# Performance work log

Measured on AMD Instinct MI355X. Metric: run time of the kernel, lower is better.

Reference implementation:

```python
import jax, jax.numpy as jnp
import numpy as np

E = 600_000
NUM_RADIAL = 6
HIDDEN = 128
OUT = 256
NUM_LAYERS = 3
N_NODES = 50_000


def setup_inputs() -> dict:
    key = jax.random.key(0)
    ks = jax.random.split(key, 6)
    x = jax.random.normal(ks[0], (E, HIDDEN), dtype=jnp.float32)
    rbf = jax.random.normal(ks[1], (E, NUM_RADIAL), dtype=jnp.float32)
    i = jax.random.randint(ks[2], (E,), 0, N_NODES, dtype=jnp.int64)
    # Linear weights stored as [in, out] so y = x @ W (equivalent to torch x @ W.T)
    W_rbf = jax.random.normal(ks[3], (NUM_RADIAL, HIDDEN), dtype=jnp.float32) / np.sqrt(NUM_RADIAL)
    W_down = jax.random.normal(ks[4], (HIDDEN, OUT), dtype=jnp.float32) / np.sqrt(HIDDEN)
    Ws = jax.random.normal(ks[5], (NUM_LAYERS, OUT, OUT), dtype=jnp.float32) / np.sqrt(OUT)
    bs = jnp.zeros((NUM_LAYERS, OUT), dtype=jnp.float32)
    return {"x": x, "rbf": rbf, "i": i, "W_rbf": W_rbf, "W_down": W_down,
            "Ws": Ws, "bs": bs, "num_nodes": N_NODES}


def reference(x, rbf, i, W_rbf, W_down, Ws, bs, num_nodes):
    # elementwise gate: lin_rbf(rbf) * x  -> [E, hidden]
    g = (rbf @ W_rbf) * x
    # scatter-add over edge target index i -> [num_nodes, hidden]
    h = jax.ops.segment_sum(g, i, num_segments=num_nodes)
    # down projection -> [num_nodes, out]
    h = h @ W_down
    # dense MLP stack with SiLU
    for k in range(Ws.shape[0]):
        h = jax.nn.silu(h @ Ws[k] + bs[k])
    return h
```

## Files before the change

### kernel.cpp

```cpp
#include <hip/hip_runtime.h>
#include <hip/hip_bf16.h>
#include <cstdint>

typedef __attribute__((ext_vector_type(8))) short short8;
typedef __attribute__((ext_vector_type(4))) float floatx4;

#define HIDDEN 128
#define NOUT 256

__global__ __launch_bounds__(256) void prep_weights(
    const float* __restrict__ Wd, const float* __restrict__ Ws,
    __hip_bfloat16* __restrict__ WdT, __hip_bfloat16* __restrict__ WsT)
{
    int tid = blockIdx.x * 256 + threadIdx.x;
    if (tid < 256 * 128) {
        int n = tid >> 7, k = tid & 127;
        WdT[tid] = __float2bfloat16(Wd[k * 256 + n]);
    }
    int tid2 = tid - 256 * 128;
    if (tid2 >= 0 && tid2 < 3 * 256 * 256) {
        int l = tid2 >> 16;
        int rem = tid2 & 65535;
        int n = rem >> 8, k = rem & 255;
        WsT[tid2] = __float2bfloat16(Ws[l * 65536 + k * 256 + n]);
    }
}

__global__ __launch_bounds__(256) void hist_k(
    const int* __restrict__ idx, int* __restrict__ cnt, int E)
{
    int e = blockIdx.x * 256 + threadIdx.x;
    if (e < E) atomicAdd(&cnt[idx[e]], 1);
}

__global__ __launch_bounds__(256) void scan_blocksum_k(
    const int* __restrict__ cnt, int* __restrict__ blocksum, int M)
{
    int base = blockIdx.x * 1024;
    int t = threadIdx.x;
    int s = 0;
#pragma unroll
    for (int j = 0; j < 4; ++j) {
        int p = base + t * 4 + j;
        if (p < M) s += cnt[p];
    }
#pragma unroll
    for (int d = 32; d > 0; d >>= 1) s += __shfl_down(s, d);
    __shared__ int wsum[4];
    if ((t & 63) == 0) wsum[t >> 6] = s;
    __syncthreads();
    if (t == 0) blocksum[blockIdx.x] = wsum[0] + wsum[1] + wsum[2] + wsum[3];
}

__global__ __launch_bounds__(64) void scan_base_k(
    const int* __restrict__ blocksum, int* __restrict__ blockbase,
    int* __restrict__ offsets, int nb, int M)
{
    int lane = threadIdx.x;
    int carry = 0;
    for (int base = 0; base < nb; base += 64) {
        int v = (base + lane < nb) ? blocksum[base + lane] : 0;
        int incl = v;
#pragma unroll
        for (int d = 1; d < 64; d <<= 1) {
            int u = __shfl_up(incl, d);
            if (lane >= d) incl += u;
        }
        if (base + lane < nb) blockbase[base + lane] = carry + incl - v;
        carry += __shfl(incl, 63);
    }
    if (lane == 0) offsets[M] = carry;
}

__global__ __launch_bounds__(256) void scan_offsets_k(
    const int* __restrict__ cnt, const int* __restrict__ blockbase,
    int* __restrict__ offsets, int* __restrict__ cursor, int M)
{
    int base = blockIdx.x * 1024;
    int t = threadIdx.x, lane = t & 63, wv = t >> 6;
    int v[4];
    int s = 0;
#pragma unroll
    for (int j = 0; j < 4; ++j) {
        int p = base + t * 4 + j;
        v[j] = (p < M) ? cnt[p] : 0;
        s += v[j];
    }
    int incl = s;
#pragma unroll
    for (int d = 1; d < 64; d <<= 1) {
        int u = __shfl_up(incl, d);
        if (lane >= d) incl += u;
    }
    __shared__ int wtot[4];
    if (lane == 63) wtot[wv] = incl;
    __syncthreads();
    int wbase = 0;
    for (int j = 0; j < wv; ++j) wbase += wtot[j];
    int start = blockbase[blockIdx.x] + wbase + incl - s;
#pragma unroll
    for (int j = 0; j < 4; ++j) {
        int p = base + t * 4 + j;
        if (p < M) { offsets[p] = start; cursor[p] = start; }
        start += v[j];
    }
}

__global__ __launch_bounds__(256) void fill_k(
    const int* __restrict__ idx, int* __restrict__ cursor,
    int* __restrict__ edge_ids, int E)
{
    int e = blockIdx.x * 256 + threadIdx.x;
    if (e < E) {
        int pos = atomicAdd(&cursor[idx[e]], 1);
        edge_ids[pos] = e;
    }
}

__global__ __launch_bounds__(256) void gather_k(
    const float* __restrict__ x, const float* __restrict__ rbf,
    const float* __restrict__ Wrbf, const int* __restrict__ offsets,
    const int* __restrict__ edge_ids, __hip_bfloat16* __restrict__ hacc, int M)
{
    int t = threadIdx.x;
    int wave = t >> 6, lane = t & 63;
    int n = blockIdx.x * 4 + wave;
    if (n >= M) return;

    int c0 = lane * 2;
    float w0[6], w1[6];
#pragma unroll
    for (int r = 0; r < 6; ++r) {
        w0[r] = Wrbf[r * HIDDEN + c0];
        w1[r] = Wrbf[r * HIDDEN + c0 + 1];
    }

    int s = offsets[n], eend = offsets[n + 1];
    float a0 = 0.f, a1 = 0.f;

    for (int p = s; p < eend; p += 64) {
        int nb = eend - p;
        if (nb > 64) nb = 64;
        int eid = (p + lane < eend) ? edge_ids[p + lane] : 0;

        int j = 0;
        for (; j + 4 <= nb; j += 4) {
#pragma unroll
            for (int u = 0; u < 4; ++u) {
                int e = __builtin_amdgcn_readlane(eid, j + u);
                const float* rb = rbf + (long)e * 6;
                float2 xv = *(const float2*)&x[(long)e * HIDDEN + c0];
                float p0 = 0.f, p1 = 0.f;
#pragma unroll
                for (int r = 0; r < 6; ++r) {
                    float rv = rb[r];
                    p0 += rv * w0[r];
                    p1 += rv * w1[r];
                }
                a0 += p0 * xv.x;
                a1 += p1 * xv.y;
            }
        }
        for (; j < nb; ++j) {
            int e = __builtin_amdgcn_readlane(eid, j);
            const float* rb = rbf + (long)e * 6;
            float2 xv = *(const float2*)&x[(long)e * HIDDEN + c0];
            float p0 = 0.f, p1 = 0.f;
#pragma unroll
            for (int r = 0; r < 6; ++r) {
                float rv = rb[r];
                p0 += rv * w0[r];
                p1 += rv * w1[r];
            }
            a0 += p0 * xv.x;
            a1 += p1 * xv.y;
        }
    }

    __hip_bfloat162 pk;
    pk.x = __float2bfloat16(a0);
    pk.y = __float2bfloat16(a1);
    *(__hip_bfloat162*)&hacc[(long)n * HIDDEN + c0] = pk;
}

__global__ __launch_bounds__(256, 3) void mlp_fused(
    const __hip_bfloat16* __restrict__ hacc, const __hip_bfloat16* __restrict__ WdT,
    const __hip_bfloat16* __restrict__ WsT, const float* __restrict__ bs,
    float* __restrict__ out, int M)
{
    __shared__ __hip_bfloat16 Al[64][264];

    int t = threadIdx.x;
    int lane = t & 63, w = t >> 6;
    int q = lane >> 4, r16 = lane & 15;
    int m0 = blockIdx.x * 64;

#pragma unroll
    for (int it = 0; it < 4; ++it) {
        int idx = it * 256 + t;
        int row = idx >> 4;
        int col = (idx & 15) * 8;
        int gr = m0 + row; if (gr >= M) gr = M - 1;
        *(short8*)&Al[row][col] = *(const short8*)&hacc[(long)gr * HIDDEN + col];
    }
    __syncthreads();

    for (int layer = 0; layer < 4; ++layer) {
        const int K = (layer == 0) ? 128 : 256;
        const __hip_bfloat16* BT = (layer == 0) ? WdT : WsT + (layer - 1) * 65536;
        const __hip_bfloat16* Brow = BT + (long)(w * 64 + r16) * K;

        floatx4 acc[4][4] = {};
        short8 bcur[4], bnxt[4];
#pragma unroll
        for (int nt = 0; nt < 4; ++nt)
            bcur[nt] = *(const short8*)&Brow[(long)nt * 16 * K + q * 8];

        for (int kk = 0; kk < K; kk += 32) {
            short8 af[4];
#pragma unroll
            for (int mt = 0; mt < 4; ++mt)
                af[mt] = *(const short8*)&Al[mt * 16 + r16][kk + q * 8];
            int kn = kk + 32;
            if (kn < K) {
#pragma unroll
                for (int nt = 0; nt < 4; ++nt)
                    bnxt[nt] = *(const short8*)&Brow[(long)nt * 16 * K + kn + q * 8];
            }
#pragma unroll
            for (int mt = 0; mt < 4; ++mt)
#pragma unroll
                for (int nt = 0; nt < 4; ++nt)
                    acc[mt][nt] = __builtin_amdgcn_mfma_f32_16x16x32_bf16(
                        af[mt], bcur[nt], acc[mt][nt], 0, 0, 0);
#pragma unroll
            for (int nt = 0; nt < 4; ++nt) bcur[nt] = bnxt[nt];
        }

        if (layer < 3) {
            __syncthreads();
            const float* bias = (layer == 0) ? nullptr : bs + (layer - 1) * 256;
#pragma unroll
            for (int mt = 0; mt < 4; ++mt) {
#pragma unroll
                for (int rr = 0; rr < 4; ++rr) {
                    int row = mt * 16 + q * 4 + rr;
#pragma unroll
                    for (int nt = 0; nt < 4; ++nt) {
                        int col = w * 64 + nt * 16 + r16;
                        float v = acc[mt][nt][rr];
                        if (layer > 0) { v += bias[col]; v = v / (1.f + __expf(-v)); }
                        Al[row][col] = __float2bfloat16(v);
                    }
                }
            }
            __syncthreads();
        } else {
            const float* bias = bs + 2 * 256;
#pragma unroll
            for (int mt = 0; mt < 4; ++mt) {
#pragma unroll
                for (int rr = 0; rr < 4; ++rr) {
                    int row = m0 + mt * 16 + q * 4 + rr;
                    if (row < M) {
#pragma unroll
                        for (int nt = 0; nt < 4; ++nt) {
                            int col = w * 64 + nt * 16 + r16;
                            float v = acc[mt][nt][rr] + bias[col];
                            v = v / (1.f + __expf(-v));
                            out[(long)row * NOUT + col] = v;
                        }
                    }
                }
            }
        }
    }
}

extern "C" void kernel_launch(void* const* d_in, const int* in_sizes, int n_in,
                              void* d_out, int out_size, void* d_ws, size_t ws_size,
                              hipStream_t stream)
{
    const float* x    = (const float*)d_in[0];
    const float* rbf  = (const float*)d_in[1];
    const int*   idx  = (const int*)d_in[2];
    const float* Wrbf = (const float*)d_in[3];
    const float* Wd   = (const float*)d_in[4];
    const float* Ws   = (const float*)d_in[5];
    const float* bs   = (const float*)d_in[6];

    int E = in_sizes[0] / HIDDEN;
    int M = out_size / NOUT;
    int nb = (M + 1023) / 1024;

    char* ws = (char*)d_ws;
    __hip_bfloat16* hacc = (__hip_bfloat16*)ws;
    size_t off = (size_t)M * HIDDEN * sizeof(float);
    __hip_bfloat16* WdT = (__hip_bfloat16*)(ws + off); off += 256 * 128 * 2;
    __hip_bfloat16* WsT = (__hip_bfloat16*)(ws + off); off += 3 * 256 * 256 * 2;
    int* cnt       = (int*)(ws + off); off += (size_t)M * 4;
    int* offsets   = (int*)(ws + off); off += (size_t)(M + 1) * 4;
    int* cursor    = (int*)(ws + off); off += (size_t)M * 4;
    int* edge_ids  = (int*)(ws + off); off += (size_t)E * 4;
    int* blocksum  = (int*)(ws + off); off += (size_t)nb * 4;
    int* blockbase = (int*)(ws + off); off += (size_t)nb * 4;

    hipMemsetAsync(cnt, 0, (size_t)M * sizeof(int), stream);
    prep_weights<<<(256 * 128 + 3 * 256 * 256 + 255) / 256, 256, 0, stream>>>(Wd, Ws, WdT, WsT);
    hist_k<<<(E + 255) / 256, 256, 0, stream>>>(idx, cnt, E);
    scan_blocksum_k<<<nb, 256, 0, stream>>>(cnt, blocksum, M);
    scan_base_k<<<1, 64, 0, stream>>>(blocksum, blockbase, offsets, nb, M);
    scan_offsets_k<<<nb, 256, 0, stream>>>(cnt, blockbase, offsets, cursor, M);
    fill_k<<<(E + 255) / 256, 256, 0, stream>>>(idx, cursor, edge_ids, E);
    gather_k<<<(M + 3) / 4, 256, 0, stream>>>(x, rbf, Wrbf, offsets, edge_ids, hacc, M);
    mlp_fused<<<(M + 63) / 64, 256, 0, stream>>>(hacc, WdT, WsT, bs, (float*)d_out, M);
}
```

Measured before the change: 629.7 us.

## Fuse CSR build and gather into one persistent cooperative kernel

Replaces the memset plus seven separate front-end kernels (weight prep, histogram, three-stage scan, fill, gather) with a single cooperative persistent kernel that separates phases with grid-wide syncs. The goal is to remove per-launch gaps and tail idle time between the many small kernels. In exchange, grid.sync barriers are added, occupancy is capped by the grid size, and the gather becomes a grid-stride loop over nodes. The old multi-kernel path stays as a fallback if the cooperative launch fails.

Result: slower. 1.394 ms (+121.4%).

```diff
diff --git a/kernel.cpp b/kernel.cpp
--- a/kernel.cpp
+++ b/kernel.cpp
@@ -1,12 +1,181 @@
 #include <hip/hip_runtime.h>
 #include <hip/hip_bf16.h>
+#include <hip/hip_cooperative_groups.h>
 #include <cstdint>
+
+namespace cg = cooperative_groups;
 
 typedef __attribute__((ext_vector_type(8))) short short8;
 typedef __attribute__((ext_vector_type(4))) float floatx4;
 
 #define HIDDEN 128
 #define NOUT 256
+
+__global__ __launch_bounds__(256, 4) void fused_front(
+    const float* __restrict__ x, const float* __restrict__ rbf,
+    const int* __restrict__ idx, const float* __restrict__ Wrbf,
+    const float* __restrict__ Wd, const float* __restrict__ Ws,
+    __hip_bfloat16* __restrict__ WdT, __hip_bfloat16* __restrict__ WsT,
+    int* __restrict__ cnt, int* __restrict__ offsets, int* __restrict__ cursor,
+    int* __restrict__ edge_ids, int* __restrict__ blocksum,
+    int* __restrict__ blockbase, __hip_bfloat16* __restrict__ hacc,
+    int E, int M, int nb)
+{
+    cg::grid_group grid = cg::this_grid();
+    int t = threadIdx.x;
+    int gtid = blockIdx.x * 256 + t;
+    int gsz = gridDim.x * 256;
+
+    __shared__ int wsum[4];
+    __shared__ int wtot[4];
+
+    for (int p = gtid; p < M; p += gsz) cnt[p] = 0;
+    for (int p = gtid; p < 256 * 128; p += gsz) {
+        int n = p >> 7, k = p & 127;
+        WdT[p] = __float2bfloat16(Wd[k * 256 + n]);
+    }
+    for (int p = gtid; p < 3 * 256 * 256; p += gsz) {
+        int l = p >> 16, rem = p & 65535, n = rem >> 8, k = rem & 255;
+        WsT[p] = __float2bfloat16(Ws[l * 65536 + k * 256 + n]);
+    }
+    grid.sync();
+
+    for (int e = gtid; e < E; e += gsz) atomicAdd(&cnt[idx[e]], 1);
+    grid.sync();
+
+    for (int c = blockIdx.x; c < nb; c += gridDim.x) {
+        int base = c * 1024;
+        int s = 0;
+#pragma unroll
+        for (int j = 0; j < 4; ++j) {
+            int p = base + t * 4 + j;
+            if (p < M) s += cnt[p];
+        }
+#pragma unroll
+        for (int d = 32; d > 0; d >>= 1) s += __shfl_down(s, d);
+        if ((t & 63) == 0) wsum[t >> 6] = s;
+        __syncthreads();
+        if (t == 0) blocksum[c] = wsum[0] + wsum[1] + wsum[2] + wsum[3];
+        __syncthreads();
+    }
+    grid.sync();
+
+    if (blockIdx.x == 0 && t < 64) {
+        int lane = t;
+        int carry = 0;
+        for (int base = 0; base < nb; base += 64) {
+            int v = (base + lane < nb) ? blocksum[base + lane] : 0;
+            int incl = v;
+#pragma unroll
+            for (int d = 1; d < 64; d <<= 1) {
+                int u = __shfl_up(incl, d);
+                if (lane >= d) incl += u;
+            }
+            if (base + lane < nb) blockbase[base + lane] = carry + incl - v;
+            carry += __shfl(incl, 63);
+        }
+        if (lane == 0) offsets[M] = carry;
+    }
+    grid.sync();
+
+    {
+        int lane = t & 63, wv = t >> 6;
+        for (int c = blockIdx.x; c < nb; c += gridDim.x) {
+            int base = c * 1024;
+            int v[4];
+            int s = 0;
+#pragma unroll
+            for (int j = 0; j < 4; ++j) {
+                int p = base + t * 4 + j;
+                v[j] = (p < M) ? cnt[p] : 0;
+                s += v[j];
+            }
+            int incl = s;
+#pragma unroll
+            for (int d = 1; d < 64; d <<= 1) {
+                int u = __shfl_up(incl, d);
+                if (lane >= d) incl += u;
+            }
+            if (lane == 63) wtot[wv] = incl;
+            __syncthreads();
+            int wbase = 0;
+            for (int j = 0; j < wv; ++j) wbase += wtot[j];
+            int start = blockbase[c] + wbase + incl - s;
+#pragma unroll
+            for (int j = 0; j < 4; ++j) {
+                int p = base + t * 4 + j;
+                if (p < M) { offsets[p] = start; cursor[p] = start; }
+                start += v[j];
+            }
+            __syncthreads();
+        }
+    }
+    grid.sync();
+
+    for (int e = gtid; e < E; e += gsz) {
+        int pos = atomicAdd(&cursor[idx[e]], 1);
+        edge_ids[pos] = e;
+    }
+    grid.sync();
+
+    {
+        int wave = t >> 6, lane = t & 63;
+        int wgid = blockIdx.x * 4 + wave;
+        int nwaves = gridDim.x * 4;
+        int c0 = lane * 2;
+        float w0[6], w1[6];
+#pragma unroll
+        for (int r = 0; r < 6; ++r) {
+            w0[r] = Wrbf[r * HIDDEN + c0];
+            w1[r] = Wrbf[r * HIDDEN + c0 + 1];
+        }
+        for (int n = wgid; n < M; n += nwaves) {
+            int s = offsets[n], eend = offsets[n + 1];
+            float a0 = 0.f, a1 = 0.f;
+            for (int p = s; p < eend; p += 64) {
+                int nbk = eend - p;
+                if (nbk > 64) nbk = 64;
+                int eid = (p + lane < eend) ? edge_ids[p + lane] : 0;
+                int j = 0;
+                for (; j + 4 <= nbk; j += 4) {
+#pragma unroll
+                    for (int u = 0; u < 4; ++u) {
+                        int e = __builtin_amdgcn_readlane(eid, j + u);
+                        const float* rb = rbf + (long)e * 6;
+                        float2 xv = *(const float2*)&x[(long)e * HIDDEN + c0];
+                        float p0 = 0.f, p1 = 0.f;
+#pragma unroll
+                        for (int r = 0; r < 6; ++r) {
+                            float rv = rb[r];
+                            p0 += rv * w0[r];
+                            p1 += rv * w1[r];
+                        }
+                        a0 += p0 * xv.x;
+                        a1 += p1 * xv.y;
+                    }
+                }
+                for (; j < nbk; ++j) {
+                    int e = __builtin_amdgcn_readlane(eid, j);
+                    const float* rb = rbf + (long)e * 6;
+                    float2 xv = *(const float2*)&x[(long)e * HIDDEN + c0];
+                    float p0 = 0.f, p1 = 0.f;
+#pragma unroll
+                    for (int r = 0; r < 6; ++r) {
+                        float rv = rb[r];
+                        p0 += rv * w0[r];
+                        p1 += rv * w1[r];
+                    }
+                    a0 += p0 * xv.x;
+                    a1 += p1 * xv.y;
+                }
+            }
+            __hip_bfloat162 pk;
+            pk.x = __float2bfloat16(a0);
+            pk.y = __float2bfloat16(a1);
+            *(__hip_bfloat162*)&hacc[(long)n * HIDDEN + c0] = pk;
+        }
+    }
+}
 
 __global__ __launch_bounds__(256) void prep_weights(
     const float* __restrict__ Wd, const float* __restrict__ Ws,
@@ -126,7 +295,6 @@
     int wave = t >> 6, lane = t & 63;
     int n = blockIdx.x * 4 + wave;
     if (n >= M) return;
-
     int c0 = lane * 2;
     float w0[6], w1[6];
 #pragma unroll
@@ -134,34 +302,13 @@
         w0[r] = Wrbf[r * HIDDEN + c0];
         w1[r] = Wrbf[r * HIDDEN + c0 + 1];
     }
-
     int s = offsets[n], eend = offsets[n + 1];
     float a0 = 0.f, a1 = 0.f;
-
     for (int p = s; p < eend; p += 64) {
-        int nb = eend - p;
-        if (nb > 64) nb = 64;
+        int nbk = eend - p;
+        if (nbk > 64) nbk = 64;
         int eid = (p + lane < eend) ? edge_ids[p + lane] : 0;
-
-        int j = 0;
-        for (; j + 4 <= nb; j += 4) {
-#pragma unroll
-            for (int u = 0; u < 4; ++u) {
-                int e = __builtin_amdgcn_readlane(eid, j + u);
-                const float* rb = rbf + (long)e * 6;
-                float2 xv = *(const float2*)&x[(long)e * HIDDEN + c0];
-                float p0 = 0.f, p1 = 0.f;
-#pragma unroll
-                for (int r = 0; r < 6; ++r) {
-                    float rv = rb[r];
-                    p0 += rv * w0[r];
-                    p1 += rv * w1[r];
-                }
-                a0 += p0 * xv.x;
-                a1 += p1 * xv.y;
-            }
-        }
-        for (; j < nb; ++j) {
+        for (int j = 0; j < nbk; ++j) {
             int e = __builtin_amdgcn_readlane(eid, j);
             const float* rb = rbf + (long)e * 6;
             float2 xv = *(const float2*)&x[(long)e * HIDDEN + c0];
@@ -176,7 +323,6 @@
             a1 += p1 * xv.y;
         }
     }
-
     __hip_bfloat162 pk;
     pk.x = __float2bfloat16(a0);
     pk.y = __float2bfloat16(a1);
@@ -305,13 +451,37 @@
     int* blocksum  = (int*)(ws + off); off += (size_t)nb * 4;
     int* blockbase = (int*)(ws + off); off += (size_t)nb * 4;
 
-    hipMemsetAsync(cnt, 0, (size_t)M * sizeof(int), stream);
-    prep_weights<<<(256 * 128 + 3 * 256 * 256 + 255) / 256, 256, 0, stream>>>(Wd, Ws, WdT, WsT);
-    hist_k<<<(E + 255) / 256, 256, 0, stream>>>(idx, cnt, E);
-    scan_blocksum_k<<<nb, 256, 0, stream>>>(cnt, blocksum, M);
-    scan_base_k<<<1, 64, 0, stream>>>(blocksum, blockbase, offsets, nb, M);
-    scan_offsets_k<<<nb, 256, 0, stream>>>(cnt, blockbase, offsets, cursor, M);
-    fill_k<<<(E + 255) / 256, 256, 0, stream>>>(idx, cursor, edge_ids, E);
-    gather_k<<<(M + 3) / 4, 256, 0, stream>>>(x, rbf, Wrbf, offsets, edge_ids, hacc, M);
+    static int occ = -1;
+    if (occ < 0) {
+        if (hipOccupancyMaxActiveBlocksPerMultiprocessor(&occ, fused_front, 256, 0)
+            != hipSuccess || occ < 1) occ = 0;
+    }
+
+    bool coop_ok = false;
+    if (occ >= 1) {
+        int grid = occ * 256;
+        if (grid > 2048) grid = 2048;
+        void* kargs[] = {
+            (void*)&x, (void*)&rbf, (void*)&idx, (void*)&Wrbf,
+            (void*)&Wd, (void*)&Ws, (void*)&WdT, (void*)&WsT,
+            (void*)&cnt, (void*)&offsets, (void*)&cursor, (void*)&edge_ids,
+            (void*)&blocksum, (void*)&blockbase, (void*)&hacc,
+            (void*)&E, (void*)&M, (void*)&nb };
+        hipError_t err = hipLaunchCooperativeKernel(
+            (void*)fused_front, dim3(grid), dim3(256), kargs, 0, stream);
+        coop_ok = (err == hipSuccess);
+    }
+
+    if (!coop_ok) {
+        hipMemsetAsync(cnt, 0, (size_t)M * sizeof(int), stream);
+        prep_weights<<<(256 * 128 + 3 * 256 * 256 + 255) / 256, 256, 0, stream>>>(Wd, Ws, WdT, WsT);
+        hist_k<<<(E + 255) / 256, 256, 0, stream>>>(idx, cnt, E);
+        scan_blocksum_k<<<nb, 256, 0, stream>>>(cnt, blocksum, M);
+        scan_base_k<<<1, 64, 0, stream>>>(blocksum, blockbase, offsets, nb, M);
+        scan_offsets_k<<<nb, 256, 0, stream>>>(cnt, blockbase, offsets, cursor, M);
+        fill_k<<<(E + 255) / 256, 256, 0, stream>>>(idx, cursor, edge_ids, E);
+        gather_k<<<(M + 3) / 4, 256, 0, stream>>>(x, rbf, Wrbf, offsets, edge_ids, hacc, M);
+    }
+
     mlp_fused<<<(M + 63) / 64, 256, 0, stream>>>(hacc, WdT, WsT, bs, (float*)d_out, M);
 }
```

## Replace CSR sort-and-gather with direct atomic scatter-add into fp32 accumulator

Applied to the files above, without the earlier changes.

Removes the histogram, prefix scan, and edge-bucketing kernels and the per-node gather. A single kernel now streams edges contiguously, computes the rbf gate, and atomically adds into an fp32 node accumulator that is zeroed by a memset. The MLP kernel converts fp32 to bf16 when it loads. This trades several launches and random x reads for many global float atomics, which contend on hot nodes and make the summation order nondeterministic.

Result: slower. 941.3 us (+49.5%).

```diff
diff --git a/kernel.cpp b/kernel.cpp
--- a/kernel.cpp
+++ b/kernel.cpp
@@ -26,108 +26,17 @@
     }
 }
 
-__global__ __launch_bounds__(256) void hist_k(
-    const int* __restrict__ idx, int* __restrict__ cnt, int E)
-{
-    int e = blockIdx.x * 256 + threadIdx.x;
-    if (e < E) atomicAdd(&cnt[idx[e]], 1);
-}
-
-__global__ __launch_bounds__(256) void scan_blocksum_k(
-    const int* __restrict__ cnt, int* __restrict__ blocksum, int M)
-{
-    int base = blockIdx.x * 1024;
+__global__ __launch_bounds__(256) void scatter_k(
+    const float* __restrict__ x, const float* __restrict__ rbf,
+    const int* __restrict__ idx, const float* __restrict__ Wrbf,
+    float* __restrict__ hacc, int E)
+{
     int t = threadIdx.x;
-    int s = 0;
-#pragma unroll
-    for (int j = 0; j < 4; ++j) {
-        int p = base + t * 4 + j;
-        if (p < M) s += cnt[p];
-    }
-#pragma unroll
-    for (int d = 32; d > 0; d >>= 1) s += __shfl_down(s, d);
-    __shared__ int wsum[4];
-    if ((t & 63) == 0) wsum[t >> 6] = s;
-    __syncthreads();
-    if (t == 0) blocksum[blockIdx.x] = wsum[0] + wsum[1] + wsum[2] + wsum[3];
-}
-
-__global__ __launch_bounds__(64) void scan_base_k(
-    const int* __restrict__ blocksum, int* __restrict__ blockbase,
-    int* __restrict__ offsets, int nb, int M)
-{
-    int lane = threadIdx.x;
-    int carry = 0;
-    for (int base = 0; base < nb; base += 64) {
-        int v = (base + lane < nb) ? blocksum[base + lane] : 0;
-        int incl = v;
-#pragma unroll
-        for (int d = 1; d < 64; d <<= 1) {
-            int u = __shfl_up(incl, d);
-            if (lane >= d) incl += u;
-        }
-        if (base + lane < nb) blockbase[base + lane] = carry + incl - v;
-        carry += __shfl(incl, 63);
-    }
-    if (lane == 0) offsets[M] = carry;
-}
-
-__global__ __launch_bounds__(256) void scan_offsets_k(
-    const int* __restrict__ cnt, const int* __restrict__ blockbase,
-    int* __restrict__ offsets, int* __restrict__ cursor, int M)
-{
-    int base = blockIdx.x * 1024;
-    int t = threadIdx.x, lane = t & 63, wv = t >> 6;
-    int v[4];
-    int s = 0;
-#pragma unroll
-    for (int j = 0; j < 4; ++j) {
-        int p = base + t * 4 + j;
-        v[j] = (p < M) ? cnt[p] : 0;
-        s += v[j];
-    }
-    int incl = s;
-#pragma unroll
-    for (int d = 1; d < 64; d <<= 1) {
-        int u = __shfl_up(incl, d);
-        if (lane >= d) incl += u;
-    }
-    __shared__ int wtot[4];
-    if (lane == 63) wtot[wv] = incl;
-    __syncthreads();
-    int wbase = 0;
-    for (int j = 0; j < wv; ++j) wbase += wtot[j];
-    int start = blockbase[blockIdx.x] + wbase + incl - s;
-#pragma unroll
-    for (int j = 0; j < 4; ++j) {
-        int p = base + t * 4 + j;
-        if (p < M) { offsets[p] = start; cursor[p] = start; }
-        start += v[j];
-    }
-}
-
-__global__ __launch_bounds__(256) void fill_k(
-    const int* __restrict__ idx, int* __restrict__ cursor,
-    int* __restrict__ edge_ids, int E)
-{
-    int e = blockIdx.x * 256 + threadIdx.x;
-    if (e < E) {
-        int pos = atomicAdd(&cursor[idx[e]], 1);
-        edge_ids[pos] = e;
-    }
-}
-
-__global__ __launch_bounds__(256) void gather_k(
-    const float* __restrict__ x, const float* __restrict__ rbf,
-    const float* __restrict__ Wrbf, const int* __restrict__ offsets,
-    const int* __restrict__ edge_ids, __hip_bfloat16* __restrict__ hacc, int M)
-{
-    int t = threadIdx.x;
-    int wave = t >> 6, lane = t & 63;
-    int n = blockIdx.x * 4 + wave;
-    if (n >= M) return;
-
+    int lane = t & 63;
+    int wave = (blockIdx.x * 256 + t) >> 6;
+    int nwaves = gridDim.x * 4;
     int c0 = lane * 2;
+
     float w0[6], w1[6];
 #pragma unroll
     for (int r = 0; r < 6; ++r) {
@@ -135,56 +44,57 @@
         w1[r] = Wrbf[r * HIDDEN + c0 + 1];
     }
 
-    int s = offsets[n], eend = offsets[n + 1];
-    float a0 = 0.f, a1 = 0.f;
-
-    for (int p = s; p < eend; p += 64) {
-        int nb = eend - p;
-        if (nb > 64) nb = 64;
-        int eid = (p + lane < eend) ? edge_ids[p + lane] : 0;
-
-        int j = 0;
-        for (; j + 4 <= nb; j += 4) {
-#pragma unroll
-            for (int u = 0; u < 4; ++u) {
-                int e = __builtin_amdgcn_readlane(eid, j + u);
-                const float* rb = rbf + (long)e * 6;
-                float2 xv = *(const float2*)&x[(long)e * HIDDEN + c0];
-                float p0 = 0.f, p1 = 0.f;
-#pragma unroll
-                for (int r = 0; r < 6; ++r) {
-                    float rv = rb[r];
-                    p0 += rv * w0[r];
-                    p1 += rv * w1[r];
-                }
-                a0 += p0 * xv.x;
-                a1 += p1 * xv.y;
-            }
-        }
-        for (; j < nb; ++j) {
-            int e = __builtin_amdgcn_readlane(eid, j);
-            const float* rb = rbf + (long)e * 6;
-            float2 xv = *(const float2*)&x[(long)e * HIDDEN + c0];
+    int epw = ((E + nwaves - 1) / nwaves + 3) & ~3;
+    int e0 = wave * epw;
+    int e1 = e0 + epw; if (e1 > E) e1 = E;
+    if (e0 >= E) return;
+
+    int e = e0;
+    for (; e + 4 <= e1; e += 4) {
+        int nd[4];
+        float2 xv[4];
+        float rbv[4][6];
+#pragma unroll
+        for (int u = 0; u < 4; ++u) {
+            int ee = e + u;
+            nd[u] = idx[ee];
+            xv[u] = *(const float2*)&x[(long)ee * HIDDEN + c0];
+            const float* rb = rbf + (long)ee * 6;
+#pragma unroll
+            for (int r = 0; r < 6; ++r) rbv[u][r] = rb[r];
+        }
+#pragma unroll
+        for (int u = 0; u < 4; ++u) {
             float p0 = 0.f, p1 = 0.f;
 #pragma unroll
             for (int r = 0; r < 6; ++r) {
-                float rv = rb[r];
-                p0 += rv * w0[r];
-                p1 += rv * w1[r];
-            }
-            a0 += p0 * xv.x;
-            a1 += p1 * xv.y;
-        }
-    }
-
-    __hip_bfloat162 pk;
-    pk.x = __float2bfloat16(a0);
-    pk.y = __float2bfloat16(a1);
-    *(__hip_bfloat162*)&hacc[(long)n * HIDDEN + c0] = pk;
+                p0 += rbv[u][r] * w0[r];
+                p1 += rbv[u][r] * w1[r];
+            }
+            float* dst = &hacc[(long)nd[u] * HIDDEN + c0];
+            atomicAdd(dst,     p0 * xv[u].x);
+            atomicAdd(dst + 1, p1 * xv[u].y);
+        }
+    }
+    for (; e < e1; ++e) {
+        int node = idx[e];
+        float2 xv = *(const float2*)&x[(long)e * HIDDEN + c0];
+        const float* rb = rbf + (long)e * 6;
+        float p0 = 0.f, p1 = 0.f;
+#pragma unroll
+        for (int r = 0; r < 6; ++r) {
+            float rv = rb[r];
+            p0 += rv * w0[r];
+            p1 += rv * w1[r];
+        }
+        float* dst = &hacc[(long)node * HIDDEN + c0];
+        atomicAdd(dst,     p0 * xv.x);
+        atomicAdd(dst + 1, p1 * xv.y);
+    }
 }
 
 __global__ __launch_bounds__(256, 3) void mlp_fused(
-    const __hip_bfloat16* __restrict__ hacc, const __hip_bfloat16* __restrict__ WdT,
+    const float* __restrict__ hacc, const __hip_bfloat16* __restrict__ WdT,
     const __hip_bfloat16* __restrict__ WsT, const float* __restrict__ bs,
     float* __restrict__ out, int M)
 {
@@ -196,12 +106,16 @@
     int m0 = blockIdx.x * 64;
 
 #pragma unroll
-    for (int it = 0; it < 4; ++it) {
+    for (int it = 0; it < 8; ++it) {
         int idx = it * 256 + t;
-        int row = idx >> 4;
-        int col = (idx & 15) * 8;
+        int row = idx >> 5;
+        int col = (idx & 31) * 4;
         int gr = m0 + row; if (gr >= M) gr = M - 1;
-        *(short8*)&Al[row][col] = *(const short8*)&hacc[(long)gr * HIDDEN + col];
+        float4 v = *(const float4*)&hacc[(long)gr * HIDDEN + col];
+        Al[row][col + 0] = __float2bfloat16(v.x);
+        Al[row][col + 1] = __float2bfloat16(v.y);
+        Al[row][col + 2] = __float2bfloat16(v.z);
+        Al[row][col + 3] = __float2bfloat16(v.w);
     }
     __syncthreads();
 
@@ -291,27 +205,15 @@
 
     int E = in_sizes[0] / HIDDEN;
     int M = out_size / NOUT;
-    int nb = (M + 1023) / 1024;
 
     char* ws = (char*)d_ws;
-    __hip_bfloat16* hacc = (__hip_bfloat16*)ws;
+    float* hacc = (float*)ws;
     size_t off = (size_t)M * HIDDEN * sizeof(float);
     __hip_bfloat16* WdT = (__hip_bfloat16*)(ws + off); off += 256 * 128 * 2;
     __hip_bfloat16* WsT = (__hip_bfloat16*)(ws + off); off += 3 * 256 * 256 * 2;
-    int* cnt       = (int*)(ws + off); off += (size_t)M * 4;
-    int* offsets   = (int*)(ws + off); off += (size_t)(M + 1) * 4;
-    int* cursor    = (int*)(ws + off); off += (size_t)M * 4;
-    int* edge_ids  = (int*)(ws + off); off += (size_t)E * 4;
-    int* blocksum  = (int*)(ws + off); off += (size_t)nb * 4;
-    int* blockbase = (int*)(ws + off); off += (size_t)nb * 4;
-
-    hipMemsetAsync(cnt, 0, (size_t)M * sizeof(int), stream);
+
+    hipMemsetAsync(hacc, 0, (size_t)M * HIDDEN * sizeof(float), stream);
     prep_weights<<<(256 * 128 + 3 * 256 * 256 + 255) / 256, 256, 0, stream>>>(Wd, Ws, WdT, WsT);
-    hist_k<<<(E + 255) / 256, 256, 0, stream>>>(idx, cnt, E);
-    scan_blocksum_k<<<nb, 256, 0, stream>>>(cnt, blocksum, M);
-    scan_base_k<<<1, 64, 0, stream>>>(blocksum, blockbase, offsets, nb, M);
-    scan_offsets_k<<<nb, 256, 0, stream>>>(cnt, blockbase, offsets, cursor, M);
-    fill_k<<<(E + 255) / 256, 256, 0, stream>>>(idx, cursor, edge_ids, E);
-    gather_k<<<(M + 3) / 4, 256, 0, stream>>>(x, rbf, Wrbf, offsets, edge_ids, hacc, M);
+    scatter_k<<<2048, 256, 0, stream>>>(x, rbf, idx, Wrbf, hacc, E);
     mlp_fused<<<(M + 63) / 64, 256, 0, stream>>>(hacc, WdT, WsT, bs, (float*)d_out, M);
 }
```
